# Performance work log

Measured on AMD Instinct MI355X. Metric: run time of the kernel, lower is better.

Reference implementation:

```python
import jax, jax.numpy as jnp
import numpy as np

EPS = 1e-6

def setup_inputs() -> dict:
    key = jax.random.key(0)
    k1, k2, k3 = jax.random.split(key, 3)
    N, L, S, H, D = 8, 4096, 4096, 8, 64
    queries = jax.random.normal(k1, (N, L, H, D), dtype=jnp.float32)
    keys = jax.random.normal(k2, (N, S, H, D), dtype=jnp.float32)
    values = jax.random.normal(k3, (N, S, H, D), dtype=jnp.float32)
    return {"queries": queries, "keys": keys, "values": values}

def reference(queries, keys, values):
    # elu(x)+1 feature maps (positive kernel)
    Q = jax.nn.elu(queries) + 1.0  # [N,L,H,D]
    K = jax.nn.elu(keys) + 1.0     # [N,S,H,D]
    v_length = values.shape[1]
    v = values / v_length          # scale for numerical stability
    # per-head KV state: [N,H,D,Dv]
    KV = jnp.einsum('nshd,nshv->nhdv', K, v)
    # normalizer: [N,L,H]
    K_sum = K.sum(axis=1)  # [N,H,D]
    Z = 1.0 / (jnp.einsum('nlhd,nhd->nlh', Q, K_sum) + EPS)
    out = jnp.einsum('nlhd,nhdv,nlh->nlhv', Q, KV, Z) * v_length
    return out
```

## Files before the change

### kernel.cpp

```cpp
#include <hip/hip_runtime.h>
#include <hip/hip_bf16.h>
#include <cstddef>
#include <cstdint>

#define N_B   8
#define L_L   4096
#define S_S   4096
#define H_H   8
#define D_D   64
#define NH    64
#define KVLD  68
#define KVSZ  (65 * KVLD)

__device__ __forceinline__ float elu1(float x) {
    return x > 0.f ? x + 1.f : __expf(x);
}

__global__ __launch_bounds__(256, 4)
void la_phase1(const float* __restrict__ Kin, const float* __restrict__ Vin,
               float* __restrict__ partials, int split, int schunk)
{
    __shared__ float sK[32 * 64];
    __shared__ float sV[32 * 64];
    __shared__ float sAcc[64 * 68];
    __shared__ float sKsumP[4 * 64];

    const int b     = blockIdx.x;
    const int nh    = b / split;
    const int chunk = b - nh * split;
    const int n     = nh >> 3;
    const int h     = nh & 7;
    const int s0    = chunk * schunk;

    const int tid  = threadIdx.x;
    const int w    = tid >> 6;
    const int lane = tid & 63;
    const int dg   = lane >> 3;
    const int vg   = lane & 7;

    float acc[8][8];
    #pragma unroll
    for (int i = 0; i < 8; ++i)
        #pragma unroll
        for (int j = 0; j < 8; ++j) acc[i][j] = 0.f;
    float ksum = 0.f;

    const int sr = tid >> 3;
    const int sc = (tid & 7) * 8;
    const int kd = lane;

    const float* Kb = Kin + (size_t)n * S_S * (H_H * D_D) + h * D_D;
    const float* Vb = Vin + (size_t)n * S_S * (H_H * D_D) + h * D_D;

    const int ntiles = schunk >> 5;
    for (int t = 0; t < ntiles; ++t) {
        const int srow = s0 + t * 32;
        {
            const float* kg = Kb + (size_t)(srow + sr) * (H_H * D_D) + sc;
            const float* vgp = Vb + (size_t)(srow + sr) * (H_H * D_D) + sc;
            float4 ka = *(const float4*)kg;
            float4 kb = *(const float4*)(kg + 4);
            float4 va = *(const float4*)vgp;
            float4 vb = *(const float4*)(vgp + 4);
            ka.x = elu1(ka.x); ka.y = elu1(ka.y); ka.z = elu1(ka.z); ka.w = elu1(ka.w);
            kb.x = elu1(kb.x); kb.y = elu1(kb.y); kb.z = elu1(kb.z); kb.w = elu1(kb.w);
            *(float4*)&sK[sr * 64 + sc]     = ka;
            *(float4*)&sK[sr * 64 + sc + 4] = kb;
            *(float4*)&sV[sr * 64 + sc]     = va;
            *(float4*)&sV[sr * 64 + sc + 4] = vb;
        }
        __syncthreads();

        #pragma unroll
        for (int sl = 0; sl < 8; ++sl) {
            const int s = w * 8 + sl;
            const float4 k0 = *(const float4*)&sK[s * 64 + dg * 8];
            const float4 k1 = *(const float4*)&sK[s * 64 + dg * 8 + 4];
            const float4 v0 = *(const float4*)&sV[s * 64 + vg * 8];
            const float4 v1 = *(const float4*)&sV[s * 64 + vg * 8 + 4];
            const float kf[8] = {k0.x, k0.y, k0.z, k0.w, k1.x, k1.y, k1.z, k1.w};
            const float vf[8] = {v0.x, v0.y, v0.z, v0.w, v1.x, v1.y, v1.z, v1.w};
            #pragma unroll
            for (int i = 0; i < 8; ++i)
                #pragma unroll
                for (int j = 0; j < 8; ++j)
                    acc[i][j] = fmaf(kf[i], vf[j], acc[i][j]);
        }
        #pragma unroll
        for (int sl = 0; sl < 8; ++sl)
            ksum += sK[(w * 8 + sl) * 64 + kd];
        __syncthreads();
    }

    for (int ww = 0; ww < 4; ++ww) {
        if (w == ww) {
            #pragma unroll
            for (int i = 0; i < 8; ++i) {
                float* p = &sAcc[(dg * 8 + i) * 68 + vg * 8];
                if (ww == 0) {
                    *(float4*)p       = make_float4(acc[i][0], acc[i][1], acc[i][2], acc[i][3]);
                    *(float4*)(p + 4) = make_float4(acc[i][4], acc[i][5], acc[i][6], acc[i][7]);
                } else {
                    float4 a0 = *(const float4*)p;
                    float4 a1 = *(const float4*)(p + 4);
                    a0.x += acc[i][0]; a0.y += acc[i][1]; a0.z += acc[i][2]; a0.w += acc[i][3];
                    a1.x += acc[i][4]; a1.y += acc[i][5]; a1.z += acc[i][6]; a1.w += acc[i][7];
                    *(float4*)p       = a0;
                    *(float4*)(p + 4) = a1;
                }
            }
        }
        __syncthreads();
    }

    sKsumP[w * 64 + kd] = ksum;
    __syncthreads();

    float* outp = partials + (size_t)b * KVSZ;
    for (int idx = tid; idx < KVSZ; idx += 256) {
        const int r = idx / KVLD;
        const int c = idx - r * KVLD;
        float val = 0.f;
        if (c < 64) {
            if (r < 64)
                val = sAcc[idx];
            else
                val = sKsumP[c] + sKsumP[64 + c] + sKsumP[128 + c] + sKsumP[192 + c];
        }
        outp[idx] = val;
    }
}

__global__ __launch_bounds__(256)
void la_reduce(const float* __restrict__ partials, float* __restrict__ kvt, int split)
{
    const int idx = blockIdx.x * 256 + threadIdx.x;
    if (idx >= NH * KVSZ) return;
    const int nh  = idx / KVSZ;
    const int rem = idx - nh * KVSZ;
    const float* p = partials + (size_t)nh * split * KVSZ + rem;
    float s = 0.f;
    for (int c = 0; c < split; ++c) s += p[(size_t)c * KVSZ];
    kvt[idx] = s;
}

__global__ __launch_bounds__(256, 2)
void la_phase2(const float* __restrict__ Qin, const float* __restrict__ kvt,
               float* __restrict__ Out)
{
    __shared__ float sQ[128 * 68];
    __shared__ float sKV[KVSZ];

    const int b   = blockIdx.x;
    const int nh  = b >> 5;
    const int lc  = b & 31;
    const int n   = nh >> 3;
    const int h   = nh & 7;
    const int tid = threadIdx.x;
    const int w    = tid >> 6;
    const int lane = tid & 63;

    const float* Qc = Qin + (((size_t)n * L_L + (size_t)lc * 128) * H_H + h) * D_D;
    float*       Oc = Out + (((size_t)n * L_L + (size_t)lc * 128) * H_H + h) * D_D;

    {
        const float4* src = (const float4*)(kvt + (size_t)nh * KVSZ);
        float4*       dst = (float4*)sKV;
        #pragma unroll
        for (int it = 0; it < 4; ++it)
            dst[it * 256 + tid] = src[it * 256 + tid];
        if (tid < 81) dst[1024 + tid] = src[1024 + tid];
    }

    #pragma unroll
    for (int it = 0; it < 8; ++it) {
        const int slot = it * 256 + tid;
        const int r    = slot >> 4;
        const int c4   = slot & 15;
        float4 v = *(const float4*)(Qc + (size_t)r * (H_H * D_D) + c4 * 4);
        v.x = elu1(v.x); v.y = elu1(v.y); v.z = elu1(v.z); v.w = elu1(v.w);
        *(float4*)&sQ[r * 68 + c4 * 4] = v;
    }
    __syncthreads();

    const int rt   = (w >> 1) * 64;
    const int wc   = w & 1;
    const int rl   = lane & 7;
    const int cg   = lane >> 3;
    const int ccol = wc * 32 + cg * 4;

    float acc[8][4];
    float den[8];
    #pragma unroll
    for (int j = 0; j < 8; ++j) {
        den[j] = 0.f;
        #pragma unroll
        for (int m = 0; m < 4; ++m) acc[j][m] = 0.f;
    }

    const int qbase = rt + rl;

    for (int kc = 0; kc < 16; ++kc) {
        float4 qv[8];
        #pragma unroll
        for (int j = 0; j < 8; ++j)
            qv[j] = *(const float4*)&sQ[(qbase + 8 * j) * 68 + kc * 4];
        const float4 kv0 = *(const float4*)&sKV[(kc * 4 + 0) * KVLD + ccol];
        const float4 kv1 = *(const float4*)&sKV[(kc * 4 + 1) * KVLD + ccol];
        const float4 kv2 = *(const float4*)&sKV[(kc * 4 + 2) * KVLD + ccol];
        const float4 kv3 = *(const float4*)&sKV[(kc * 4 + 3) * KVLD + ccol];
        const float4 ks  = *(const float4*)&sKV[64 * KVLD + kc * 4];

        #pragma unroll
        for (int j = 0; j < 8; ++j) {
            const float q0 = qv[j].x, q1 = qv[j].y, q2 = qv[j].z, q3 = qv[j].w;
            den[j] = fmaf(q0, ks.x, den[j]);
            den[j] = fmaf(q1, ks.y, den[j]);
            den[j] = fmaf(q2, ks.z, den[j]);
            den[j] = fmaf(q3, ks.w, den[j]);
            acc[j][0] = fmaf(q0, kv0.x, acc[j][0]);
            acc[j][0] = fmaf(q1, kv1.x, acc[j][0]);
            acc[j][0] = fmaf(q2, kv2.x, acc[j][0]);
            acc[j][0] = fmaf(q3, kv3.x, acc[j][0]);
            acc[j][1] = fmaf(q0, kv0.y, acc[j][1]);
            acc[j][1] = fmaf(q1, kv1.y, acc[j][1]);
            acc[j][1] = fmaf(q2, kv2.y, acc[j][1]);
            acc[j][1] = fmaf(q3, kv3.y, acc[j][1]);
            acc[j][2] = fmaf(q0, kv0.z, acc[j][2]);
            acc[j][2] = fmaf(q1, kv1.z, acc[j][2]);
            acc[j][2] = fmaf(q2, kv2.z, acc[j][2]);
            acc[j][2] = fmaf(q3, kv3.z, acc[j][2]);
            acc[j][3] = fmaf(q0, kv0.w, acc[j][3]);
            acc[j][3] = fmaf(q1, kv1.w, acc[j][3]);
            acc[j][3] = fmaf(q2, kv2.w, acc[j][3]);
            acc[j][3] = fmaf(q3, kv3.w, acc[j][3]);
        }
    }

    #pragma unroll
    for (int j = 0; j < 8; ++j) {
        const float rz = 1.0f / (den[j] + 1e-6f);
        *(float4*)(Oc + (size_t)(qbase + 8 * j) * (H_H * D_D) + ccol) =
            make_float4(acc[j][0] * rz, acc[j][1] * rz,
                        acc[j][2] * rz, acc[j][3] * rz);
    }
}

extern "C" void kernel_launch(void* const* d_in, const int* in_sizes, int n_in,
                              void* d_out, int out_size, void* d_ws, size_t ws_size,
                              hipStream_t stream)
{
    const float* Q = (const float*)d_in[0];
    const float* K = (const float*)d_in[1];
    const float* V = (const float*)d_in[2];
    float* out = (float*)d_out;

    float* kvt = (float*)d_ws;
    const size_t kvt_bytes = (size_t)NH * KVSZ * sizeof(float);

    int split = 16;
    while (split > 1 &&
           kvt_bytes + (size_t)NH * split * KVSZ * sizeof(float) > ws_size)
        split >>= 1;
    float* partials = kvt + (size_t)NH * KVSZ;
    const int schunk = S_S / split;

    la_phase1<<<NH * split, 256, 0, stream>>>(K, V, partials, split, schunk);

    const int red_blocks = (NH * KVSZ + 255) / 256;
    la_reduce<<<red_blocks, 256, 0, stream>>>(partials, kvt, split);

    la_phase2<<<NH * (L_L / 128), 256, 0, stream>>>(Q, kvt, out);
}
```

Measured before the change: 99.16 us.

## Give each wave private K/V rows, load V direct to LDS, drop barriers

The KV accumulation kernel now stages 64-row tiles in which each wave loads and consumes only its own 16 rows. That removes both per-tile __syncthreads. V is copied straight from global memory into LDS with global_load_lds, and K still goes through registers so the elu transform can be applied. The staging buffers share a union with the reduction buffer, and the launch-bounds occupancy hint drops from 4 to 3. In exchange it relies on an explicit vmcnt wait, implicit intra-wave LDS ordering, and a larger shared footprint per block.

```diff
diff --git a/kernel.cpp b/kernel.cpp
--- a/kernel.cpp
+++ b/kernel.cpp
@@ -12,17 +12,21 @@
 #define KVLD  68
 #define KVSZ  (65 * KVLD)
 
+typedef const float __attribute__((address_space(1)))* gas_fp;
+typedef float __attribute__((address_space(3)))* las_fp;
+
 __device__ __forceinline__ float elu1(float x) {
     return x > 0.f ? x + 1.f : __expf(x);
 }
 
-__global__ __launch_bounds__(256, 4)
+__global__ __launch_bounds__(256, 3)
 void la_phase1(const float* __restrict__ Kin, const float* __restrict__ Vin,
                float* __restrict__ partials, int split, int schunk)
 {
-    __shared__ float sK[32 * 64];
-    __shared__ float sV[32 * 64];
-    __shared__ float sAcc[64 * 68];
+    __shared__ union {
+        struct { float K[64 * 64]; float V[64 * 64]; } st;
+        float acc[64 * 68];
+    } sm;
     __shared__ float sKsumP[4 * 64];
 
     const int b     = blockIdx.x;
@@ -45,39 +49,47 @@
         for (int j = 0; j < 8; ++j) acc[i][j] = 0.f;
     float ksum = 0.f;
 
-    const int sr = tid >> 3;
-    const int sc = (tid & 7) * 8;
-    const int kd = lane;
+    const int ksr = tid >> 2;
+    const int ksc = (tid & 3) * 16;
+    const int kd  = lane;
+
+    const int vr = lane >> 4;
+    const int vc = (lane & 15) * 4;
 
     const float* Kb = Kin + (size_t)n * S_S * (H_H * D_D) + h * D_D;
     const float* Vb = Vin + (size_t)n * S_S * (H_H * D_D) + h * D_D;
 
-    const int ntiles = schunk >> 5;
+    const int ntiles = schunk >> 6;
+
     for (int t = 0; t < ntiles; ++t) {
-        const int srow = s0 + t * 32;
-        {
-            const float* kg = Kb + (size_t)(srow + sr) * (H_H * D_D) + sc;
-            const float* vgp = Vb + (size_t)(srow + sr) * (H_H * D_D) + sc;
-            float4 ka = *(const float4*)kg;
-            float4 kb = *(const float4*)(kg + 4);
-            float4 va = *(const float4*)vgp;
-            float4 vb = *(const float4*)(vgp + 4);
-            ka.x = elu1(ka.x); ka.y = elu1(ka.y); ka.z = elu1(ka.z); ka.w = elu1(ka.w);
-            kb.x = elu1(kb.x); kb.y = elu1(kb.y); kb.z = elu1(kb.z); kb.w = elu1(kb.w);
-            *(float4*)&sK[sr * 64 + sc]     = ka;
-            *(float4*)&sK[sr * 64 + sc + 4] = kb;
-            *(float4*)&sV[sr * 64 + sc]     = va;
-            *(float4*)&sV[sr * 64 + sc + 4] = vb;
-        }
-        __syncthreads();
-
-        #pragma unroll
-        for (int sl = 0; sl < 8; ++sl) {
-            const int s = w * 8 + sl;
-            const float4 k0 = *(const float4*)&sK[s * 64 + dg * 8];
-            const float4 k1 = *(const float4*)&sK[s * 64 + dg * 8 + 4];
-            const float4 v0 = *(const float4*)&sV[s * 64 + vg * 8];
-            const float4 v1 = *(const float4*)&sV[s * 64 + vg * 8 + 4];
+        const int srow = s0 + t * 64;
+
+        #pragma unroll
+        for (int c = 0; c < 4; ++c) {
+            const int ch = w * 4 + c;
+            __builtin_amdgcn_global_load_lds(
+                (gas_fp)(Vb + (size_t)(srow + ch * 4 + vr) * (H_H * D_D) + vc),
+                (las_fp)&sm.st.V[ch * 256], 16, 0, 0);
+        }
+
+        #pragma unroll
+        for (int p = 0; p < 4; ++p) {
+            float4 kv = *(const float4*)(Kb + (size_t)(srow + ksr) * (H_H * D_D)
+                                         + ksc + p * 4);
+            kv.x = elu1(kv.x); kv.y = elu1(kv.y);
+            kv.z = elu1(kv.z); kv.w = elu1(kv.w);
+            *(float4*)&sm.st.K[ksr * 64 + ksc + p * 4] = kv;
+        }
+
+        asm volatile("s_waitcnt vmcnt(0)" ::: "memory");
+
+        #pragma unroll 4
+        for (int sl = 0; sl < 16; ++sl) {
+            const int s = w * 16 + sl;
+            const float4 k0 = *(const float4*)&sm.st.K[s * 64 + dg * 8];
+            const float4 k1 = *(const float4*)&sm.st.K[s * 64 + dg * 8 + 4];
+            const float4 v0 = *(const float4*)&sm.st.V[s * 64 + vg * 8];
+            const float4 v1 = *(const float4*)&sm.st.V[s * 64 + vg * 8 + 4];
             const float kf[8] = {k0.x, k0.y, k0.z, k0.w, k1.x, k1.y, k1.z, k1.w};
             const float vf[8] = {v0.x, v0.y, v0.z, v0.w, v1.x, v1.y, v1.z, v1.w};
             #pragma unroll
@@ -87,16 +99,16 @@
                     acc[i][j] = fmaf(kf[i], vf[j], acc[i][j]);
         }
         #pragma unroll
-        for (int sl = 0; sl < 8; ++sl)
-            ksum += sK[(w * 8 + sl) * 64 + kd];
-        __syncthreads();
-    }
+        for (int sl = 0; sl < 16; ++sl)
+            ksum += sm.st.K[(w * 16 + sl) * 64 + kd];
+    }
+    __syncthreads();
 
     for (int ww = 0; ww < 4; ++ww) {
         if (w == ww) {
             #pragma unroll
             for (int i = 0; i < 8; ++i) {
-                float* p = &sAcc[(dg * 8 + i) * 68 + vg * 8];
+                float* p = &sm.acc[(dg * 8 + i) * 68 + vg * 8];
                 if (ww == 0) {
                     *(float4*)p       = make_float4(acc[i][0], acc[i][1], acc[i][2], acc[i][3]);
                     *(float4*)(p + 4) = make_float4(acc[i][4], acc[i][5], acc[i][6], acc[i][7]);
@@ -123,7 +135,7 @@
         float val = 0.f;
         if (c < 64) {
             if (r < 64)
-                val = sAcc[idx];
+                val = sm.acc[idx];
             else
                 val = sKsumP[c] + sKsumP[64 + c] + sKsumP[128 + c] + sKsumP[192 + c];
         }
```

Result: slower. 106.1 us (+7.0%).

## Compute KV outer-product accumulation with bf16 MFMA and double-buffered transposed tiles

Applied to the files above, without the earlier changes.

Replaces the scalar FP32 FMA outer-product in phase 1 with bf16 MFMA 16x16x32 instructions. K and V tiles are converted to bf16 and stored transposed in double-buffered LDS, and the next tile's global loads are issued before the current tile's compute. The K column sum is folded into an extra MFMA against a vector of ones, and the cross-wave LDS reduction is dropped because each wave now owns distinct output rows. This lowers ALU cost and synchronisation, but bf16 rounding of K and V reduces precision.

```diff
diff --git a/kernel.cpp b/kernel.cpp
--- a/kernel.cpp
+++ b/kernel.cpp
@@ -11,19 +11,30 @@
 #define NH    64
 #define KVLD  68
 #define KVSZ  (65 * KVLD)
+#define ROWF  (H_H * D_D)
+#define TSTEP (32 * ROWF)
+#define KTLD  40
+
+typedef float f32x4 __attribute__((ext_vector_type(4)));
+typedef short bf16x8 __attribute__((ext_vector_type(8)));
 
 __device__ __forceinline__ float elu1(float x) {
     return x > 0.f ? x + 1.f : __expf(x);
+}
+
+__device__ __forceinline__ void wr_pair(short* base, int d, int p, float a, float b) {
+    *reinterpret_cast<__hip_bfloat162*>(&base[d * KTLD + 2 * p]) =
+        __float22bfloat162_rn(make_float2(a, b));
 }
 
 __global__ __launch_bounds__(256, 4)
 void la_phase1(const float* __restrict__ Kin, const float* __restrict__ Vin,
                float* __restrict__ partials, int split, int schunk)
 {
-    __shared__ float sK[32 * 64];
-    __shared__ float sV[32 * 64];
-    __shared__ float sAcc[64 * 68];
-    __shared__ float sKsumP[4 * 64];
+    __shared__ union {
+        struct { short Kt[2][64 * KTLD]; short Vt[2][64 * KTLD]; } st;
+        float acc[64 * 68];
+    } sm;
 
     const int b     = blockIdx.x;
     const int nh    = b / split;
@@ -35,85 +46,91 @@
     const int tid  = threadIdx.x;
     const int w    = tid >> 6;
     const int lane = tid & 63;
-    const int dg   = lane >> 3;
-    const int vg   = lane & 7;
-
-    float acc[8][8];
-    #pragma unroll
-    for (int i = 0; i < 8; ++i)
-        #pragma unroll
-        for (int j = 0; j < 8; ++j) acc[i][j] = 0.f;
-    float ksum = 0.f;
-
-    const int sr = tid >> 3;
-    const int sc = (tid & 7) * 8;
-    const int kd = lane;
-
-    const float* Kb = Kin + (size_t)n * S_S * (H_H * D_D) + h * D_D;
-    const float* Vb = Vin + (size_t)n * S_S * (H_H * D_D) + h * D_D;
+    const int a2   = lane & 15;
+    const int kg   = lane >> 4;
+
+    const int p  = tid >> 4;
+    const int c4 = (tid & 15) * 4;
+
+    f32x4 acc[4];
+    f32x4 acck;
+    const f32x4 z4 = {0.f, 0.f, 0.f, 0.f};
+    acck = z4;
+    #pragma unroll
+    for (int nn = 0; nn < 4; ++nn) acc[nn] = z4;
+    const bf16x8 ones = {0x3F80, 0x3F80, 0x3F80, 0x3F80,
+                         0x3F80, 0x3F80, 0x3F80, 0x3F80};
+
+    const size_t base = (size_t)n * S_S * ROWF + h * D_D;
+    const float* kpe = Kin + base + (size_t)(s0 + 2 * p) * ROWF + c4;
+    const float* kpo = kpe + ROWF;
+    const float* vpe = Vin + base + (size_t)(s0 + 2 * p) * ROWF + c4;
+    const float* vpo = vpe + ROWF;
 
     const int ntiles = schunk >> 5;
+
+    float4 ka, kb, va, vb;
+
+#define LOADT()                                                              \
+    do {                                                                     \
+        ka = *(const float4*)kpe;  kb = *(const float4*)kpo;                 \
+        va = *(const float4*)vpe;  vb = *(const float4*)vpo;                 \
+        kpe += TSTEP; kpo += TSTEP; vpe += TSTEP; vpo += TSTEP;              \
+    } while (0)
+
+#define WRITET(BUF)                                                          \
+    do {                                                                     \
+        short* kt_ = sm.st.Kt[BUF];  short* vt_ = sm.st.Vt[BUF];             \
+        wr_pair(kt_, c4 + 0, p, elu1(ka.x), elu1(kb.x));                     \
+        wr_pair(kt_, c4 + 1, p, elu1(ka.y), elu1(kb.y));                     \
+        wr_pair(kt_, c4 + 2, p, elu1(ka.z), elu1(kb.z));                     \
+        wr_pair(kt_, c4 + 3, p, elu1(ka.w), elu1(kb.w));                     \
+        wr_pair(vt_, c4 + 0, p, va.x, vb.x);                                 \
+        wr_pair(vt_, c4 + 1, p, va.y, vb.y);                                 \
+        wr_pair(vt_, c4 + 2, p, va.z, vb.z);                                 \
+        wr_pair(vt_, c4 + 3, p, va.w, vb.w);                                 \
+    } while (0)
+
+    LOADT();
+    WRITET(0);
+    __syncthreads();
+
     for (int t = 0; t < ntiles; ++t) {
-        const int srow = s0 + t * 32;
+        const bool more = (t + 1 < ntiles);
+
+        if (more) LOADT();
+
         {
-            const float* kg = Kb + (size_t)(srow + sr) * (H_H * D_D) + sc;
-            const float* vgp = Vb + (size_t)(srow + sr) * (H_H * D_D) + sc;
-            float4 ka = *(const float4*)kg;
-            float4 kb = *(const float4*)(kg + 4);
-            float4 va = *(const float4*)vgp;
-            float4 vb = *(const float4*)(vgp + 4);
-            ka.x = elu1(ka.x); ka.y = elu1(ka.y); ka.z = elu1(ka.z); ka.w = elu1(ka.w);
-            kb.x = elu1(kb.x); kb.y = elu1(kb.y); kb.z = elu1(kb.z); kb.w = elu1(kb.w);
-            *(float4*)&sK[sr * 64 + sc]     = ka;
-            *(float4*)&sK[sr * 64 + sc + 4] = kb;
-            *(float4*)&sV[sr * 64 + sc]     = va;
-            *(float4*)&sV[sr * 64 + sc + 4] = vb;
+            const short* kt = sm.st.Kt[t & 1];
+            const short* vt = sm.st.Vt[t & 1];
+            const bf16x8 af = *(const bf16x8*)&kt[(w * 16 + a2) * KTLD + kg * 8];
+            const bf16x8 b0 = *(const bf16x8*)&vt[(0 * 16 + a2) * KTLD + kg * 8];
+            const bf16x8 b1 = *(const bf16x8*)&vt[(1 * 16 + a2) * KTLD + kg * 8];
+            const bf16x8 b2 = *(const bf16x8*)&vt[(2 * 16 + a2) * KTLD + kg * 8];
+            const bf16x8 b3 = *(const bf16x8*)&vt[(3 * 16 + a2) * KTLD + kg * 8];
+            acc[0] = __builtin_amdgcn_mfma_f32_16x16x32_bf16(af, b0, acc[0], 0, 0, 0);
+            acc[1] = __builtin_amdgcn_mfma_f32_16x16x32_bf16(af, b1, acc[1], 0, 0, 0);
+            acc[2] = __builtin_amdgcn_mfma_f32_16x16x32_bf16(af, b2, acc[2], 0, 0, 0);
+            acc[3] = __builtin_amdgcn_mfma_f32_16x16x32_bf16(af, b3, acc[3], 0, 0, 0);
+            acck   = __builtin_amdgcn_mfma_f32_16x16x32_bf16(af, ones, acck, 0, 0, 0);
         }
+
+        if (more) WRITET((t + 1) & 1);
         __syncthreads();
-
-        #pragma unroll
-        for (int sl = 0; sl < 8; ++sl) {
-            const int s = w * 8 + sl;
-            const float4 k0 = *(const float4*)&sK[s * 64 + dg * 8];
-            const float4 k1 = *(const float4*)&sK[s * 64 + dg * 8 + 4];
-            const float4 v0 = *(const float4*)&sV[s * 64 + vg * 8];
-            const float4 v1 = *(const float4*)&sV[s * 64 + vg * 8 + 4];
-            const float kf[8] = {k0.x, k0.y, k0.z, k0.w, k1.x, k1.y, k1.z, k1.w};
-            const float vf[8] = {v0.x, v0.y, v0.z, v0.w, v1.x, v1.y, v1.z, v1.w};
-            #pragma unroll
-            for (int i = 0; i < 8; ++i)
-                #pragma unroll
-                for (int j = 0; j < 8; ++j)
-                    acc[i][j] = fmaf(kf[i], vf[j], acc[i][j]);
-        }
-        #pragma unroll
-        for (int sl = 0; sl < 8; ++sl)
-            ksum += sK[(w * 8 + sl) * 64 + kd];
-        __syncthreads();
-    }
-
-    for (int ww = 0; ww < 4; ++ww) {
-        if (w == ww) {
-            #pragma unroll
-            for (int i = 0; i < 8; ++i) {
-                float* p = &sAcc[(dg * 8 + i) * 68 + vg * 8];
-                if (ww == 0) {
-                    *(float4*)p       = make_float4(acc[i][0], acc[i][1], acc[i][2], acc[i][3]);
-                    *(float4*)(p + 4) = make_float4(acc[i][4], acc[i][5], acc[i][6], acc[i][7]);
-                } else {
-                    float4 a0 = *(const float4*)p;
-                    float4 a1 = *(const float4*)(p + 4);
-                    a0.x += acc[i][0]; a0.y += acc[i][1]; a0.z += acc[i][2]; a0.w += acc[i][3];
-                    a1.x += acc[i][4]; a1.y += acc[i][5]; a1.z += acc[i][6]; a1.w += acc[i][7];
-                    *(float4*)p       = a0;
-                    *(float4*)(p + 4) = a1;
-                }
-            }
-        }
-        __syncthreads();
-    }
-
-    sKsumP[w * 64 + kd] = ksum;
+    }
+#undef LOADT
+#undef WRITET
+
+    #pragma unroll
+    for (int nn = 0; nn < 4; ++nn)
+        #pragma unroll
+        for (int r = 0; r < 4; ++r)
+            sm.acc[(w * 16 + kg * 4 + r) * 68 + nn * 16 + a2] = acc[nn][r];
+    if (a2 == 0) {
+        #pragma unroll
+        for (int r = 0; r < 4; ++r)
+            sm.acc[(w * 16 + kg * 4 + r) * 68 + 64] = acck[r];
+    }
     __syncthreads();
 
     float* outp = partials + (size_t)b * KVSZ;
@@ -123,9 +140,9 @@
         float val = 0.f;
         if (c < 64) {
             if (r < 64)
-                val = sAcc[idx];
+                val = sm.acc[idx];
             else
-                val = sKsumP[c] + sKsumP[64 + c] + sKsumP[128 + c] + sKsumP[192 + c];
+                val = sm.acc[c * 68 + 64];
         }
         outp[idx] = val;
     }
```

Result: faster. 83.73 us (-15.6%).
